# Optimization experiments

Hardware: AMD Instinct MI355X
Metric: run time of the kernel (lower is better)

The kernel has to match this reference:

```python
import jax, jax.numpy as jnp
import numpy as np
import math

N_LEVELS = 16
F_PER = 2
LOG2T = 19
TABLE = 1 << LOG2T  # 524288
BASE = 16
FINEST = 512
BANDS = 10
TIME = 0.0

_B = math.exp((math.log(FINEST) - math.log(BASE)) / (N_LEVELS - 1))
_RES = [min(int(BASE * _B ** l), FINEST) for l in range(N_LEVELS)]
# primes reduced mod table size: (c*p) mod M == (c*(p mod M)) mod M, keeps products in int32 range
_PRIMES_MOD = np.array([73856093 % TABLE, 19349663 % TABLE, 83492791 % TABLE], dtype=np.int32)
_OFFSETS = np.array([[dx, dy, dz] for dx in (0, 1) for dy in (0, 1) for dz in (0, 1)], dtype=bool)  # [8,3]


def _hash_encode(x, tables):
    # x: [N,3] in [0,1]; tables: [L, 2^19, 2]
    x = jnp.clip(x, 0.0, 1.0)
    offs = jnp.asarray(_OFFSETS)[:, None, :]  # [8,1,3]
    pm = jnp.asarray(_PRIMES_MOD)
    outs = []
    for l in range(N_LEVELS):
        res = _RES[l]
        sc = x * (res - 1)                                   # [N,3]
        cf = jnp.clip(jnp.floor(sc).astype(jnp.int32), 0, res - 1)
        cc = jnp.clip(cf + 1, 0, res - 1)
        w = sc - cf.astype(sc.dtype)                         # trilinear weights [N,3]
        corner = jnp.where(offs, cc[None], cf[None])         # [8,N,3]
        h = ((corner[..., 0] * pm[0]) % TABLE
             + (corner[..., 1] * pm[1]) % TABLE
             + (corner[..., 2] * pm[2]) % TABLE) % TABLE     # [8,N]
        feats = tables[l][h]                                 # gather [8,N,2]
        cw = jnp.prod(jnp.where(offs, w[None], 1.0 - w[None]), axis=-1)  # [8,N]
        outs.append(jnp.sum(feats * cw[..., None], axis=0))  # [N,2]
    return jnp.concatenate(outs, axis=1)                     # [N,32]


def _freq_encode(freq):
    nf = (jnp.log10(jnp.clip(freq, 1e6, 1e12)) - 6.0) / 6.0  # [N,1]
    parts = []
    for i in range(BANDS):
        a = (2.0 ** i) * math.pi * nf
        parts += [jnp.sin(a), jnp.cos(a)]
    return jnp.concatenate(parts, axis=-1)                   # [N,20]


def _ln(x, g, b, eps=1e-5):
    m = jnp.mean(x, -1, keepdims=True)
    v = jnp.var(x, -1, keepdims=True)
    return (x - m) / jnp.sqrt(v + eps) * g + b


def _forward(x, frequency, tables, W0, b0, W1, b1, W2, b2, W3, b3,
             e_w1, e_b1, e_g, e_be, e_w2, e_b2,
             m_w1, m_b1, m_g, m_be, m_w2, m_b2,
             p_w1, p_b1, p_w2, p_b2,
             mat_w1, mat_b1, mat_w2, mat_b2,
             s_w1, s_b1, s_w2, s_b2):
    pe = _hash_encode(x, tables)                             # [N,32]
    fe = _freq_encode(frequency)                             # [N,20]
    feat0 = jnp.concatenate([pe, fe], axis=1)                # [N,52]
    h = jax.nn.relu(feat0 @ W0 + b0)
    h = jax.nn.relu(h @ W1 + b1)
    h = jax.nn.relu(jnp.concatenate([h, feat0], axis=1) @ W2 + b2)  # skip connection
    h = jax.nn.relu(h @ W3 + b3)
    E_amp = jnp.tanh(jax.nn.relu(_ln(h @ e_w1 + e_b1, e_g, e_be)) @ e_w2 + e_b2)
    B_amp = jnp.tanh(jax.nn.relu(_ln(h @ m_w1 + m_b1, m_g, m_be)) @ m_w2 + m_b2)
    phases = jax.nn.relu(h @ p_w1 + p_b1) @ p_w2 + p_b2      # [N,6]
    mat = jax.nn.relu(h @ mat_w1 + mat_b1) @ mat_w2 + mat_b2 # [N,3]
    src = jax.nn.relu(h @ s_w1 + s_b1) @ s_w2 + s_b2         # [N,4]
    omega = 2.0 * math.pi * frequency                        # [N,1]
    E = E_amp * jnp.cos(omega * TIME + phases[:, :3])
    B = B_amp * jnp.cos(omega * TIME + phases[:, 3:])
    eps_r = 1.0 + jax.nn.sigmoid(mat[:, 0:1]) * 10.0
    mu_r = 1.0 + jax.nn.sigmoid(mat[:, 1:2]) * 2.0
    cond = jax.nn.sigmoid(mat[:, 2:3]) * 0.01
    # pack all float outputs: E(3) B(3) eps(1) mu(1) cond(1) charge(1) current(3)
    return jnp.concatenate([E, B, eps_r, mu_r, cond, src[:, 0:1], src[:, 1:4]], axis=1)


def _lin_init(k, fan_in, fan_out):
    k1, k2 = jax.random.split(k)
    s = 1.0 / math.sqrt(fan_in)
    W = jax.random.uniform(k1, (fan_in, fan_out), jnp.float32, -s, s)
    b = jax.random.uniform(k2, (fan_out,), jnp.float32, -s, s)
    return W, b


def setup_inputs() -> dict:
    key = jax.random.key(0)
    ks = jax.random.split(key, 20)
    N = 262144
    d = {}
    d['x'] = jax.random.uniform(ks[0], (N, 3), jnp.float32)
    d['frequency'] = 10.0 ** jax.random.uniform(ks[1], (N, 1), jnp.float32, minval=6.0, maxval=12.0)
    d['tables'] = jax.random.normal(ks[2], (N_LEVELS, TABLE, F_PER), jnp.float32) * 1e-4
    layers = [('W0', 'b0', 52, 128), ('W1', 'b1', 128, 128), ('W2', 'b2', 180, 128), ('W3', 'b3', 128, 128),
              ('e_w1', 'e_b1', 128, 64), ('e_w2', 'e_b2', 64, 3),
              ('m_w1', 'm_b1', 128, 64), ('m_w2', 'm_b2', 64, 3),
              ('p_w1', 'p_b1', 128, 32), ('p_w2', 'p_b2', 32, 6),
              ('mat_w1', 'mat_b1', 128, 64), ('mat_w2', 'mat_b2', 64, 3),
              ('s_w1', 's_b1', 128, 64), ('s_w2', 's_b2', 64, 4)]
    for j, (wn, bn, fi, fo) in enumerate(layers):
        W, b = _lin_init(jax.random.fold_in(ks[3], j), fi, fo)
        d[wn] = W
        d[bn] = b
    d['e_g'] = jnp.ones(64, jnp.float32)
    d['e_be'] = jnp.zeros(64, jnp.float32)
    d['m_g'] = jnp.ones(64, jnp.float32)
    d['m_be'] = jnp.zeros(64, jnp.float32)
    return d


def reference(x, frequency, tables, W0, b0, W1, b1, W2, b2, W3, b3,
              e_w1, e_b1, e_g, e_be, e_w2, e_b2,
              m_w1, m_b1, m_g, m_be, m_w2, m_b2,
              p_w1, p_b1, p_w2, p_b2,
              mat_w1, mat_b1, mat_w2, mat_b2,
              s_w1, s_b1, s_w2, s_b2):
    return _forward(x, frequency, tables, W0, b0, W1, b1, W2, b2, W3, b3,
                    e_w1, e_b1, e_g, e_be, e_w2, e_b2,
                    m_w1, m_b1, m_g, m_be, m_w2, m_b2,
                    p_w1, p_b1, p_w2, p_b2,
                    mat_w1, mat_b1, mat_w2, mat_b2,
                    s_w1, s_b1, s_w2, s_b2)
```

## Files before the change

kernel.cpp:

```cpp
#include <hip/hip_runtime.h>
#include <math.h>

#define TMASK 524287
#define PM0 455773
#define PM1 475295
#define PM2 130999

typedef __attribute__((ext_vector_type(8))) short bf16x8;
typedef __attribute__((ext_vector_type(4))) float f32x4;

#define OFF_W0   0
#define OFF_W1   8192
#define OFF_W2   24576
#define OFF_W3   49152
#define OFF_E    65536
#define OFF_P    81920
#define OFF_MAT  86016
#define OFF_S    94208
#define OFF_BD   102400
#define WT_TOTAL 102400
#define WT_ALLOC 111616

#define WS_TAB8_OFF (WT_ALLOC*2)
#define TAB8_BYTES  (16u*524288u*2u)
#define WS_FEAT_OFF (WS_TAB8_OFF + TAB8_BYTES)

#define TAB_SCALE   131072.0f
#define TAB_INV     (1.0f/131072.0f)

#define A6_H    0
#define A6_HL   8704
#define A6_FB   8704
#define SWF6_OFF 17408
#define LDS6_TOTAL 21712

#define SB0 0
#define SB1 128
#define SB2 256
#define SB3 384
#define SEM 512
#define SPB 640
#define SMS 672
#define SB2C 800
#define SEG 819
#define SEBE 883
#define SMG 947
#define SMBE 1011

struct Params {
  const float* x; const float* freq; const float* tables;
  const float* b0; const float* b1; const float* b2; const float* b3;
  const float* e_b1; const float* e_w2; const float* e_b2; const float* e_g; const float* e_be;
  const float* m_b1; const float* m_w2; const float* m_b2; const float* m_g; const float* m_be;
  const float* p_b1; const float* p_w2; const float* p_b2;
  const float* mat_b1; const float* mat_w2; const float* mat_b2;
  const float* s_b1; const float* s_w2; const float* s_b2;
  const short* wt;
  const unsigned* feat;
  float* out;
  int N;
  int res[16];
  const float* ssrc[18]; int sdst[18]; int scnt[18];
};

struct HashParams {
  const float* x; const unsigned short* tab8; unsigned* feat; int N; int res[16];
};
struct TabPrepParams { const float* tables; unsigned* tab8; };
struct PrepParams {
  const float* src[9];
  int end[9]; int Nsrc[9]; int Ksrc[9]; int Kpad[9];
  short* wt;
};
struct BdParams {
  const float* e; const float* m; const float* p; const float* mat; const float* s;
  short* out;
};

__device__ __forceinline__ short f2bf(float f){
  union { float f; unsigned u; } v; v.f = f;
  unsigned r = v.u + 0x7fffu + ((v.u >> 16) & 1u);
  return (short)(r >> 16);
}
__device__ __forceinline__ float bf2f(short s){
  union { unsigned u; float f; } v; v.u = ((unsigned)(unsigned short)s) << 16; return v.f;
}
__device__ __forceinline__ float sigmoid_(float v){ return 1.f/(1.f + expf(-v)); }

__global__ __launch_bounds__(256)
void prep_weights(PrepParams P)
{
  int id = blockIdx.x*256 + threadIdx.x;
  if (id >= WT_TOTAL) return;
  int r = 0, base = 0;
  #pragma unroll
  for (int i = 0; i < 9; ++i) { if (id >= P.end[i]) { r = i+1; base = P.end[i]; } }
  const int rel = id - base;
  const int kp = P.Kpad[r];
  const int n = rel / kp;
  const int k = rel - n*kp;
  float v = 0.f;
  if (k < P.Ksrc[r]) v = P.src[r][k * P.Nsrc[r] + n];
  P.wt[id] = f2bf(v);
}

__global__ __launch_bounds__(256)
void prep_bd(BdParams P)
{
  int id = blockIdx.x*256 + threadIdx.x;
  if (id >= 32*288) return;
  const int n = id / 288, k = id - n*288;
  float v = 0.f;
  if      (n < 3  && k < 64)                        v = P.e[k*3 + n];
  else if (n >= 3 && n < 6  && k >= 64  && k < 128) v = P.m[(k-64)*3 + (n-3)];
  else if (n >= 6 && n < 12 && k >= 256)            v = P.p[(k-256)*6 + (n-6)];
  else if (n >= 12&& n < 15 && k >= 128 && k < 192) v = P.mat[(k-128)*3 + (n-12)];
  else if (n >= 15&& n < 19 && k >= 192 && k < 256) v = P.s[(k-192)*4 + (n-15)];
  P.out[id] = f2bf(v);
}

__global__ __launch_bounds__(256)
void tab_prep(TabPrepParams P)
{
  const unsigned id = blockIdx.x*256 + threadIdx.x;
  if (id >= 16u*524288u/2u) return;
  const float4 v = ((const float4*)P.tables)[id];
  int q0 = (int)fminf(fmaxf(rintf(v.x*TAB_SCALE), -127.f), 127.f);
  int q1 = (int)fminf(fmaxf(rintf(v.y*TAB_SCALE), -127.f), 127.f);
  int q2 = (int)fminf(fmaxf(rintf(v.z*TAB_SCALE), -127.f), 127.f);
  int q3 = (int)fminf(fmaxf(rintf(v.w*TAB_SCALE), -127.f), 127.f);
  unsigned pack = (q0 & 255) | ((q1 & 255) << 8) | ((q2 & 255) << 16) | ((q3 & 255) << 24);
  P.tab8[id] = pack;
}

__global__ __launch_bounds__(256, 8)
void hash_encode8(HashParams P)
{
  const int b = blockIdx.x;
  const int l = b & 15;
  const int p = (b >> 4)*256 + threadIdx.x;
  if (p >= P.N) return;
  const float xs0 = fminf(fmaxf(P.x[p*3+0], 0.f), 1.f);
  const float xs1 = fminf(fmaxf(P.x[p*3+1], 0.f), 1.f);
  const float xs2 = fminf(fmaxf(P.x[p*3+2], 0.f), 1.f);
  const int res = P.res[l];
  const float rf = (float)(res-1);
  const float s0 = xs0*rf, s1 = xs1*rf, s2 = xs2*rf;
  int f0i = (int)s0; if (f0i > res-1) f0i = res-1;
  int f1i = (int)s1; if (f1i > res-1) f1i = res-1;
  int f2i = (int)s2; if (f2i > res-1) f2i = res-1;
  const float w0 = s0 - (float)f0i;
  const float w1 = s1 - (float)f1i;
  const float w2 = s2 - (float)f2i;
  int c0i = f0i+1; if (c0i > res-1) c0i = res-1;
  int c1i = f1i+1; if (c1i > res-1) c1i = res-1;
  int c2i = f2i+1; if (c2i > res-1) c2i = res-1;
  const int hx0 = (f0i*PM0) & TMASK, hx1 = (c0i*PM0) & TMASK;
  const int hy0 = (f1i*PM1) & TMASK, hy1 = (c1i*PM1) & TMASK;
  const int hz0 = (f2i*PM2) & TMASK, hz1 = (c2i*PM2) & TMASK;
  const unsigned short* tp = P.tab8 + ((size_t)l << 19);
  unsigned short tv[8];
  #pragma unroll
  for (int cn = 0; cn < 8; ++cn) {
    const int bx = (cn>>2)&1, by = (cn>>1)&1, bz = cn&1;
    const int hh = ((bx?hx1:hx0) + (by?hy1:hy0) + (bz?hz1:hz0)) & TMASK;
    tv[cn] = tp[hh];
  }
  float a0 = 0.f, a1 = 0.f;
  #pragma unroll
  for (int cn = 0; cn < 8; ++cn) {
    const int bx = (cn>>2)&1, by = (cn>>1)&1, bz = cn&1;
    const float cw = (bx?w0:1.f-w0)*(by?w1:1.f-w1)*(bz?w2:1.f-w2);
    a0 = fmaf(cw, (float)(int)(signed char)(tv[cn] & 0xff), a0);
    a1 = fmaf(cw, (float)(int)(signed char)(tv[cn] >> 8),   a1);
  }
  a0 *= TAB_INV; a1 *= TAB_INV;
  const unsigned pack = (unsigned)(unsigned short)f2bf(a0)
                      | ((unsigned)(unsigned short)f2bf(a1) << 16);
  P.feat[(size_t)p*16 + l] = pack;
}

template<int NT, int KC>
__device__ __forceinline__ void gemm32(f32x4* acc0, f32x4* acc1,
    const short* A, int lda, const short* __restrict__ wt, int kpad, int kwoff,
    int n0, int q)
{
  const short* Ap0 = A + n0*lda + q*8;
  const short* Ap1 = Ap0 + 16*lda;
  const short* Bp  = wt + n0*kpad + kwoff + q*8;
  bf16x8 bc[NT], bn[NT];
  #pragma unroll
  for (int nt = 0; nt < NT; ++nt) bc[nt] = *(const bf16x8*)(Bp + nt*16*kpad);
  #pragma unroll
  for (int kc = 0; kc < KC; ++kc) {
    if (kc + 1 < KC) {
      #pragma unroll
      for (int nt = 0; nt < NT; ++nt)
        bn[nt] = *(const bf16x8*)(Bp + nt*16*kpad + (kc+1)*32);
    }
    const bf16x8 a0 = *(const bf16x8*)(Ap0 + kc*32);
    const bf16x8 a1 = *(const bf16x8*)(Ap1 + kc*32);
    #pragma unroll
    for (int nt = 0; nt < NT; ++nt) {
      acc0[nt] = __builtin_amdgcn_mfma_f32_16x16x32_bf16(a0, bc[nt], acc0[nt], 0, 0, 0);
      acc1[nt] = __builtin_amdgcn_mfma_f32_16x16x32_bf16(a1, bc[nt], acc1[nt], 0, 0, 0);
    }
    #pragma unroll
    for (int nt = 0; nt < NT; ++nt) bc[nt] = bn[nt];
  }
}

template<int NT>
__device__ __forceinline__ void epi_trunk(const f32x4* acc0, const f32x4* acc1,
    const float* bias, short* out, int ldo, int n0, int q, int coff)
{
  #pragma unroll
  for (int nt = 0; nt < NT; ++nt) {
    const float bv = bias[nt*16 + n0];
    #pragma unroll
    for (int r = 0; r < 4; ++r) {
      float v0 = fmaxf(acc0[nt][r] + bv, 0.f);
      float v1 = fmaxf(acc1[nt][r] + bv, 0.f);
      out[(q*4 + r)*ldo + coff + nt*16 + n0]      = f2bf(v0);
      out[(16 + q*4 + r)*ldo + coff + nt*16 + n0] = f2bf(v1);
    }
  }
}

__global__ __launch_bounds__(128, 4)
void em_nerf6(Params P)
{
  __shared__ __align__(16) char smem[LDS6_TOTAL];
  const int tid = threadIdx.x;
  const int lane = tid & 63, wave = tid >> 6;
  short* H  = (short*)(smem + A6_H);
  short* HL = (short*)(smem + A6_HL);
  short* FB = (short*)(smem + A6_FB);
  float* R2 = (float*)(smem + A6_HL);
  float* swf = (float*)(smem + SWF6_OFF);
  const int n0 = lane & 15, q = lane >> 4;
  const int p0 = blockIdx.x*32;

  uint4 fv;
  { const int pl = tid >> 2, lq = tid & 3;
    int gp = p0 + pl; if (gp >= P.N) gp = P.N - 1;
    fv = *(const uint4*)(P.feat + (size_t)gp*16 + lq*4); }

  #pragma clang loop unroll(disable)
  for (int r = 0; r < 18; ++r)
    for (int i = tid; i < P.scnt[r]; i += 128) swf[P.sdst[r] + i] = P.ssrc[r][i];

  { const int pl = tid >> 2, lq = tid & 3;
    *(uint4*)&FB[pl*72 + lq*8] = fv; }

  { const int pp = tid & 31, half = tid >> 5;
    int gp = p0 + pp; if (gp >= P.N) gp = P.N - 1;
    float fr = P.freq[gp];
    fr = fminf(fmaxf(fr, 1e6f), 1e12f);
    const float nf = (log10f(fr) - 6.f) * (1.f/6.f);
    const float a0 = 3.14159274101257324f * nf;
    #pragma clang loop unroll(disable)
    for (int i = half; i < 10; i += 4) {
      const float a = a0 * (float)(1 << i);
      FB[pp*72 + 32 + 2*i] = f2bf(sinf(a));
      FB[pp*72 + 33 + 2*i] = f2bf(cosf(a));
    }
    if (half == 3) {
      #pragma unroll
      for (int k = 52; k < 64; ++k) FB[pp*72 + k] = 0;
    }
  }
  __syncthreads();

  const int ntb = wave*64;

  { f32x4 a0[4] = {}, a1[4] = {};
    gemm32<4,2>(a0, a1, FB, 72, P.wt + OFF_W0 + ntb*64, 64, 0, n0, q);
    epi_trunk<4>(a0, a1, swf + SB0 + ntb, H, 136, n0, q, ntb);
    __syncthreads(); }
  { f32x4 a0[4] = {}, a1[4] = {};
    gemm32<4,4>(a0, a1, H, 136, P.wt + OFF_W1 + ntb*128, 128, 0, n0, q);
    __syncthreads();
    epi_trunk<4>(a0, a1, swf + SB1 + ntb, H, 136, n0, q, ntb);
    __syncthreads(); }
  { f32x4 a0[4] = {}, a1[4] = {};
    gemm32<4,4>(a0, a1, H, 136, P.wt + OFF_W2 + ntb*192, 192, 0, n0, q);
    gemm32<4,2>(a0, a1, FB, 72, P.wt + OFF_W2 + ntb*192, 192, 128, n0, q);
    __syncthreads();
    epi_trunk<4>(a0, a1, swf + SB2 + ntb, H, 136, n0, q, ntb);
    __syncthreads(); }
  { f32x4 a0[4] = {}, a1[4] = {};
    gemm32<4,4>(a0, a1, H, 136, P.wt + OFF_W3 + ntb*128, 128, 0, n0, q);
    __syncthreads();
    epi_trunk<4>(a0, a1, swf + SB3 + ntb, H, 136, n0, q, ntb);
    __syncthreads(); }

  { f32x4 a0[4] = {}, a1[4] = {};
    gemm32<4,4>(a0, a1, H, 136, P.wt + OFF_E + ntb*128, 128, 0, n0, q);
    const float* bb = swf + SEM + ntb;
    #pragma unroll
    for (int nt = 0; nt < 4; ++nt) {
      const float bv = bb[nt*16 + n0];
      #pragma unroll
      for (int r = 0; r < 4; ++r) { a0[nt][r] += bv; a1[nt][r] += bv; }
    }
    float mn[2][4], iv[2][4];
    #pragma unroll
    for (int s = 0; s < 2; ++s) {
      const f32x4* A_ = s ? a1 : a0;
      #pragma unroll
      for (int r = 0; r < 4; ++r) {
        float se = 0.f, qe = 0.f;
        #pragma unroll
        for (int t = 0; t < 4; ++t) { const float x = A_[t][r]; se += x; qe = fmaf(x,x,qe); }
        #pragma unroll
        for (int msk = 1; msk < 16; msk <<= 1) {
          se += __shfl_xor(se, msk, 64);
          qe += __shfl_xor(qe, msk, 64);
        }
        const float me = se*(1.f/64.f);
        mn[s][r] = me;
        iv[s][r] = 1.f / sqrtf(qe*(1.f/64.f) - me*me + 1e-5f);
      }
    }
    const float* gg  = swf + (wave ? SMG  : SEG);
    const float* bbe = swf + (wave ? SMBE : SEBE);
    #pragma unroll
    for (int t = 0; t < 4; ++t) {
      const float g  = gg[t*16 + n0];
      const float be = bbe[t*16 + n0];
      const int col = ntb + t*16 + n0;
      #pragma unroll
      for (int s = 0; s < 2; ++s) {
        const f32x4* A_ = s ? a1 : a0;
        #pragma unroll
        for (int r = 0; r < 4; ++r) {
          float v = (A_[t][r] - mn[s][r])*iv[s][r]*g + be;
          v = fmaxf(v, 0.f);
          HL[(s*16 + q*4 + r)*136 + col] = f2bf(v);
        }
      }
    }
  }
  __syncthreads();

  f32x4 o0[1] = {}, o1[1] = {};
  gemm32<1,4>(o0, o1, HL, 136, P.wt + OFF_BD + wave*16*288, 288, 0, n0, q);

  { f32x4 a0[4] = {}, a1[4] = {};
    gemm32<4,4>(a0, a1, H, 136, P.wt + OFF_MAT + ntb*128, 128, 0, n0, q);
    __syncthreads();
    const float* bb = swf + SMS + ntb;
    #pragma unroll
    for (int t = 0; t < 4; ++t) {
      const float bv = bb[t*16 + n0];
      const int col = ntb + t*16 + n0;
      #pragma unroll
      for (int s = 0; s < 2; ++s) {
        const f32x4* A_ = s ? a1 : a0;
        #pragma unroll
        for (int r = 0; r < 4; ++r)
          HL[(s*16 + q*4 + r)*136 + col] = f2bf(fmaxf(A_[t][r] + bv, 0.f));
      }
    }
  }
  __syncthreads();

  gemm32<1,4>(o0, o1, HL, 136, P.wt + OFF_BD + wave*16*288, 288, 128, n0, q);

  { f32x4 a0[1] = {}, a1[1] = {};
    gemm32<1,4>(a0, a1, H, 136, P.wt + OFF_P + wave*16*128, 128, 0, n0, q);
    __syncthreads();
    const float bv = swf[SPB + wave*16 + n0];
    const int col = wave*16 + n0;
    #pragma unroll
    for (int s = 0; s < 2; ++s) {
      const f32x4* A_ = s ? a1 : a0;
      #pragma unroll
      for (int r = 0; r < 4; ++r)
        HL[(s*16 + q*4 + r)*136 + col] = f2bf(fmaxf(A_[s? 0:0][r] + bv, 0.f));
    }
  }
  __syncthreads();

  gemm32<1,1>(o0, o1, HL, 136, P.wt + OFF_BD + wave*16*288, 288, 256, n0, q);
  __syncthreads();

  #pragma unroll
  for (int s = 0; s < 2; ++s) {
    const f32x4* O_ = s ? o1 : o0;
    #pragma unroll
    for (int r = 0; r < 4; ++r) {
      const int p = s*16 + q*4 + r;
      if (wave == 0) {
        float v0 = O_[0][r] + swf[SB2C + n0];
        if (n0 < 6) v0 = tanhf(v0);
        R2[p*20 + n0] = v0;
      } else if (n0 < 3) {
        R2[p*20 + 16 + n0] = O_[0][r] + swf[SB2C + 16 + n0];
      }
    }
  }
  __syncthreads();

  if (tid < 32) {
    const int gp = p0 + tid;
    if (gp < P.N) {
      const float* r = R2 + tid*20;
      float* o = P.out + (size_t)gp*13;
      o[0] = r[0]*cosf(r[6]);
      o[1] = r[1]*cosf(r[7]);
      o[2] = r[2]*cosf(r[8]);
      o[3] = r[3]*cosf(r[9]);
      o[4] = r[4]*cosf(r[10]);
      o[5] = r[5]*cosf(r[11]);
      o[6] = 1.f + sigmoid_(r[12])*10.f;
      o[7] = 1.f + sigmoid_(r[13])*2.f;
      o[8] = sigmoid_(r[14])*0.01f;
      o[9]  = r[15];
      o[10] = r[16];
      o[11] = r[17];
      o[12] = r[18];
    }
  }
}

__global__ __launch_bounds__(256, 3)
void em_nerf_fallback(Params P)
{
  __shared__ __align__(16) char smem[44288];
  short* featB = (short*)smem;
  short* hA    = (short*)(smem + 9216);
  short* hB    = (short*)(smem + 9216 + 17664);
  float* headF = (float*)(smem + 9216);
  float* res2  = (float*)smem;
  __shared__ int s_res[16];

  const int tid = threadIdx.x;
  if (tid < 16) s_res[tid] = P.res[tid];
  __syncthreads();
  {
    const int p = tid & 63;
    const int g = tid >> 6;
    int gp = blockIdx.x*64 + p; if (gp >= P.N) gp = P.N - 1;
    const float xs0 = fminf(fmaxf(P.x[gp*3+0], 0.f), 1.f);
    const float xs1 = fminf(fmaxf(P.x[gp*3+1], 0.f), 1.f);
    const float xs2 = fminf(fmaxf(P.x[gp*3+2], 0.f), 1.f);
    #pragma unroll
    for (int j = 0; j < 4; ++j) {
      const int l = g*4 + j;
      const int res = s_res[l];
      const float rf = (float)(res-1);
      const float s0 = xs0*rf, s1 = xs1*rf, s2 = xs2*rf;
      int f0i = (int)s0; if (f0i > res-1) f0i = res-1;
      int f1i = (int)s1; if (f1i > res-1) f1i = res-1;
      int f2i = (int)s2; if (f2i > res-1) f2i = res-1;
      const float w0 = s0 - (float)f0i;
      const float w1 = s1 - (float)f1i;
      const float w2 = s2 - (float)f2i;
      int c0i = f0i+1; if (c0i > res-1) c0i = res-1;
      int c1i = f1i+1; if (c1i > res-1) c1i = res-1;
      int c2i = f2i+1; if (c2i > res-1) c2i = res-1;
      const int hx0 = (f0i*PM0) & TMASK, hx1 = (c0i*PM0) & TMASK;
      const int hy0 = (f1i*PM1) & TMASK, hy1 = (c1i*PM1) & TMASK;
      const int hz0 = (f2i*PM2) & TMASK, hz1 = (c2i*PM2) & TMASK;
      const float* tp = P.tables + ((size_t)l << 20);
      float a0 = 0.f, a1 = 0.f;
      #pragma unroll
      for (int cn = 0; cn < 8; ++cn) {
        const int bx = (cn>>2)&1, by = (cn>>1)&1, bz = cn&1;
        const int hh = ((bx?hx1:hx0) + (by?hy1:hy0) + (bz?hz1:hz0)) & TMASK;
        const float cw = (bx?w0:1.f-w0)*(by?w1:1.f-w1)*(bz?w2:1.f-w2);
        const float2 tv = *(const float2*)(tp + 2*hh);
        a0 = fmaf(cw, tv.x, a0);
        a1 = fmaf(cw, tv.y, a1);
      }
      featB[p*72 + 2*l]   = f2bf(a0);
      featB[p*72 + 2*l+1] = f2bf(a1);
    }
    if (g == 0) {
      float fr = P.freq[gp];
      fr = fminf(fmaxf(fr, 1e6f), 1e12f);
      const float nf = (log10f(fr) - 6.f) * (1.f/6.f);
      float a = 3.14159274101257324f * nf;
      #pragma unroll
      for (int i = 0; i < 10; ++i) {
        featB[p*72 + 32 + 2*i] = f2bf(sinf(a));
        featB[p*72 + 33 + 2*i] = f2bf(cosf(a));
        a = a * 2.f;
      }
    }
    if (g == 3) {
      #pragma unroll
      for (int k = 52; k < 64; ++k) featB[p*72 + k] = 0;
    }
  }
  __syncthreads();

  const int lane = tid & 63, wave = tid >> 6;
  const int n0 = lane & 15, q = lane >> 4;
  short* myA  = featB + wave*16*72;
  short* myH1 = hA + wave*16*136;
  short* myH2 = hB + wave*16*136;

  auto gemm1 = [&](const short* A, int lda, const short* wt, int kpad, int kwoff, int KC, f32x4* acc, int NT){
    const short* Ap = A + n0*lda + q*8;
    const short* Bp = wt + n0*kpad + kwoff + q*8;
    for (int kc = 0; kc < KC; ++kc) {
      bf16x8 a = *(const bf16x8*)(Ap + kc*32);
      for (int nt = 0; nt < NT; ++nt) {
        bf16x8 b = *(const bf16x8*)(Bp + nt*16*kpad + kc*32);
        acc[nt] = __builtin_amdgcn_mfma_f32_16x16x32_bf16(a, b, acc[nt], 0, 0, 0);
      }
    }
  };
  auto epi1 = [&](const f32x4* acc, const float* bias, short* out, int ldo, int NT, bool relu){
    for (int nt = 0; nt < NT; ++nt) {
      const float bv = bias[nt*16 + n0];
      for (int r = 0; r < 4; ++r) {
        float v = acc[nt][r] + bv;
        if (relu) v = fmaxf(v, 0.f);
        out[(q*4 + r)*ldo + nt*16 + n0] = f2bf(v);
      }
    }
  };

  { f32x4 acc[8] = {}; gemm1(myA, 72, P.wt + OFF_W0, 64, 0, 2, acc, 8);  epi1(acc, P.b0, myH1, 136, 8, true); }
  __syncthreads();
  { f32x4 acc[8] = {}; gemm1(myH1, 136, P.wt + OFF_W1, 128, 0, 4, acc, 8); epi1(acc, P.b1, myH2, 136, 8, true); }
  __syncthreads();
  { f32x4 acc[8] = {}; gemm1(myH2, 136, P.wt + OFF_W2, 192, 0, 4, acc, 8);
    gemm1(myA, 72, P.wt + OFF_W2, 192, 128, 2, acc, 8); epi1(acc, P.b2, myH1, 136, 8, true); }
  __syncthreads();
  { f32x4 acc[8] = {}; gemm1(myH1, 136, P.wt + OFF_W3, 128, 0, 4, acc, 8); epi1(acc, P.b3, myH2, 136, 8, true); }
  __syncthreads();

  float* hf = headF + wave*16*69;
  auto head1f = [&](const short* wt, const float* bias, int NT, bool relu){
    f32x4 acc[4] = {};
    gemm1(myH2, 136, wt, 128, 0, 4, acc, NT);
    for (int nt = 0; nt < NT; ++nt) {
      const float bv = bias[nt*16 + n0];
      for (int r = 0; r < 4; ++r) {
        float v = acc[nt][r] + bv;
        if (relu) v = fmaxf(v, 0.f);
        hf[(q*4 + r)*69 + nt*16 + n0] = v;
      }
    }
  };
  auto l2 = [&](int OC2, int K2, bool ln, bool th, const float* g, const float* be,
                const float* W2, const float* b2, int slot){
    __syncthreads();
    if (tid < 64) {
      const float* row = headF + tid*69;
      float mn = 0.f, iv = 1.f;
      if (ln) {
        float s = 0.f;
        for (int k = 0; k < K2; ++k) s += row[k];
        mn = s/(float)K2;
        float vv = 0.f;
        for (int k = 0; k < K2; ++k) { float d = row[k]-mn; vv = fmaf(d,d,vv); }
        iv = 1.f/sqrtf(vv/(float)K2 + 1e-5f);
      }
      for (int j = 0; j < OC2; ++j) {
        float acc = b2[j];
        for (int k = 0; k < K2; ++k) {
          float xv = row[k];
          if (ln) xv = (xv-mn)*iv*g[k] + be[k];
          xv = fmaxf(xv, 0.f);
          acc = fmaf(xv, W2[k*OC2+j], acc);
        }
        res2[tid*20 + slot + j] = th ? tanhf(acc) : acc;
      }
    }
    __syncthreads();
  };

  head1f(P.wt + OFF_E, P.e_b1, 4, false); l2(3, 64, true,  true,  P.e_g, P.e_be, P.e_w2, P.e_b2, 0);
  head1f(P.wt + OFF_E + 8192, P.m_b1, 4, false); l2(3, 64, true, true, P.m_g, P.m_be, P.m_w2, P.m_b2, 3);
  head1f(P.wt + OFF_P, P.p_b1, 2, true);  l2(6, 32, false, false, 0, 0, P.p_w2, P.p_b2, 6);
  head1f(P.wt + OFF_MAT, P.mat_b1, 4, true); l2(3, 64, false, false, 0, 0, P.mat_w2, P.mat_b2, 12);
  head1f(P.wt + OFF_S, P.s_b1, 4, true);  l2(4, 64, false, false, 0, 0, P.s_w2, P.s_b2, 15);

  if (tid < 64) {
    const int gp = blockIdx.x*64 + tid;
    if (gp < P.N) {
      const float* r = res2 + tid*20;
      float* o = P.out + (size_t)gp*13;
      o[0] = r[0]*cosf(r[6]);
      o[1] = r[1]*cosf(r[7]);
      o[2] = r[2]*cosf(r[8]);
      o[3] = r[3]*cosf(r[9]);
      o[4] = r[4]*cosf(r[10]);
      o[5] = r[5]*cosf(r[11]);
      o[6] = 1.f + sigmoid_(r[12])*10.f;
      o[7] = 1.f + sigmoid_(r[13])*2.f;
      o[8] = sigmoid_(r[14])*0.01f;
      o[9]  = r[15];
      o[10] = r[16];
      o[11] = r[17];
      o[12] = r[18];
    }
  }
}

extern "C" void kernel_launch(void* const* d_in, const int* in_sizes, int n_in,
                              void* d_out, int out_size, void* d_ws, size_t ws_size,
                              hipStream_t stream) {
  (void)n_in; (void)out_size;
  const float** in = (const float**)d_in;
  const int N = in_sizes[0] / 3;

  PrepParams PP;
  const float* srcs[9] = { in[3], in[5], in[7], in[9], in[11], in[15], in[19], in[23], in[27] };
  const int ends[9]  = { 8192, 24576, 49152, 65536, 73728, 81920, 86016, 94208, 102400 };
  const int nsrc[9]  = { 128, 128, 128, 128, 64, 64, 32, 64, 64 };
  const int ksrc[9]  = { 52, 128, 180, 128, 128, 128, 128, 128, 128 };
  const int kpad[9]  = { 64, 128, 192, 128, 128, 128, 128, 128, 128 };
  for (int i = 0; i < 9; ++i) { PP.src[i]=srcs[i]; PP.end[i]=ends[i]; PP.Nsrc[i]=nsrc[i]; PP.Ksrc[i]=ksrc[i]; PP.Kpad[i]=kpad[i]; }
  PP.wt = (short*)d_ws;
  hipLaunchKernelGGL(prep_weights, dim3((WT_TOTAL+255)/256), dim3(256), 0, stream, PP);

  BdParams BP;
  BP.e = in[13]; BP.m = in[17]; BP.p = in[21]; BP.mat = in[25]; BP.s = in[29];
  BP.out = (short*)d_ws + OFF_BD;
  hipLaunchKernelGGL(prep_bd, dim3((32*288 + 255)/256), dim3(256), 0, stream, BP);

  Params P;
  P.x = in[0]; P.freq = in[1]; P.tables = in[2];
  P.b0 = in[4]; P.b1 = in[6]; P.b2 = in[8]; P.b3 = in[10];
  P.e_b1 = in[12]; P.e_w2 = in[13]; P.e_b2 = in[14];
  P.m_b1 = in[16]; P.m_w2 = in[17]; P.m_b2 = in[18];
  P.p_b1 = in[20]; P.p_w2 = in[21]; P.p_b2 = in[22];
  P.mat_b1 = in[24]; P.mat_w2 = in[25]; P.mat_b2 = in[26];
  P.s_b1 = in[28]; P.s_w2 = in[29]; P.s_b2 = in[30];
  P.e_g = in[31]; P.e_be = in[32]; P.m_g = in[33]; P.m_be = in[34];
  P.wt = (const short*)d_ws;
  P.feat = (const unsigned*)((const char*)d_ws + WS_FEAT_OFF);
  P.out = (float*)d_out;
  P.N = N;

  const float* ssrc[18] = { in[4], in[6], in[8], in[10],
                            in[12], in[16], in[20], in[24], in[28],
                            in[14], in[18], in[22], in[26], in[30],
                            in[31], in[32], in[33], in[34] };
  const int sdst[18] = { 0,128,256,384, 512,576,640,672,736, 800,803,806,812,815, 819,883,947,1011 };
  const int scnt[18] = { 128,128,128,128, 64,64,32,64,64, 3,3,6,3,4, 64,64,64,64 };
  for (int i = 0; i < 18; ++i) { P.ssrc[i]=ssrc[i]; P.sdst[i]=sdst[i]; P.scnt[i]=scnt[i]; }

  const double B = exp((log(512.0) - log(16.0)) / 15.0);
  for (int l = 0; l < 16; ++l) {
    double r = 16.0 * pow(B, (double)l);
    int ri = (int)r;
    if (ri > 512) ri = 512;
    P.res[l] = ri;
  }

  const size_t need = (size_t)WS_FEAT_OFF + (size_t)N*16*4;

  if (ws_size >= need) {
    TabPrepParams TP;
    TP.tables = in[2];
    TP.tab8 = (unsigned*)((char*)d_ws + WS_TAB8_OFF);
    hipLaunchKernelGGL(tab_prep, dim3((16*524288/2 + 255)/256), dim3(256), 0, stream, TP);

    HashParams HP;
    HP.x = in[0];
    HP.tab8 = (const unsigned short*)((const char*)d_ws + WS_TAB8_OFF);
    HP.feat = (unsigned*)((char*)d_ws + WS_FEAT_OFF);
    HP.N = N;
    for (int l = 0; l < 16; ++l) HP.res[l] = P.res[l];
    const int chunks = (N + 255) / 256;
    hipLaunchKernelGGL(hash_encode8, dim3(chunks*16), dim3(256), 0, stream, HP);

    hipLaunchKernelGGL(em_nerf6, dim3((N + 31) / 32), dim3(128), 0, stream, P);
  } else {
    hipLaunchKernelGGL(em_nerf_fallback, dim3((N + 63) / 64), dim3(256), 0, stream, P);
  }
}
```

Before: 539.3 us.

## Fuse hash-grid encoding into the MLP kernel and drop the feature buffer

```diff
diff --git a/kernel.cpp b/kernel.cpp
--- a/kernel.cpp
+++ b/kernel.cpp
@@ -23,7 +23,6 @@
 
 #define WS_TAB8_OFF (WT_ALLOC*2)
 #define TAB8_BYTES  (16u*524288u*2u)
-#define WS_FEAT_OFF (WS_TAB8_OFF + TAB8_BYTES)
 
 #define TAB_SCALE   131072.0f
 #define TAB_INV     (1.0f/131072.0f)
@@ -56,16 +55,13 @@
   const float* mat_b1; const float* mat_w2; const float* mat_b2;
   const float* s_b1; const float* s_w2; const float* s_b2;
   const short* wt;
-  const unsigned* feat;
+  const unsigned short* tab8;
   float* out;
   int N;
   int res[16];
   const float* ssrc[18]; int sdst[18]; int scnt[18];
 };
 
-struct HashParams {
-  const float* x; const unsigned short* tab8; unsigned* feat; int N; int res[16];
-};
 struct TabPrepParams { const float* tables; unsigned* tab8; };
 struct PrepParams {
   const float* src[9];
@@ -133,53 +129,6 @@
   P.tab8[id] = pack;
 }
 
-__global__ __launch_bounds__(256, 8)
-void hash_encode8(HashParams P)
-{
-  const int b = blockIdx.x;
-  const int l = b & 15;
-  const int p = (b >> 4)*256 + threadIdx.x;
-  if (p >= P.N) return;
-  const float xs0 = fminf(fmaxf(P.x[p*3+0], 0.f), 1.f);
-  const float xs1 = fminf(fmaxf(P.x[p*3+1], 0.f), 1.f);
-  const float xs2 = fminf(fmaxf(P.x[p*3+2], 0.f), 1.f);
-  const int res = P.res[l];
-  const float rf = (float)(res-1);
-  const float s0 = xs0*rf, s1 = xs1*rf, s2 = xs2*rf;
-  int f0i = (int)s0; if (f0i > res-1) f0i = res-1;
-  int f1i = (int)s1; if (f1i > res-1) f1i = res-1;
-  int f2i = (int)s2; if (f2i > res-1) f2i = res-1;
-  const float w0 = s0 - (float)f0i;
-  const float w1 = s1 - (float)f1i;
-  const float w2 = s2 - (float)f2i;
-  int c0i = f0i+1; if (c0i > res-1) c0i = res-1;
-  int c1i = f1i+1; if (c1i > res-1) c1i = res-1;
-  int c2i = f2i+1; if (c2i > res-1) c2i = res-1;
-  const int hx0 = (f0i*PM0) & TMASK, hx1 = (c0i*PM0) & TMASK;
-  const int hy0 = (f1i*PM1) & TMASK, hy1 = (c1i*PM1) & TMASK;
-  const int hz0 = (f2i*PM2) & TMASK, hz1 = (c2i*PM2) & TMASK;
-  const unsigned short* tp = P.tab8 + ((size_t)l << 19);
-  unsigned short tv[8];
-  #pragma unroll
-  for (int cn = 0; cn < 8; ++cn) {
-    const int bx = (cn>>2)&1, by = (cn>>1)&1, bz = cn&1;
-    const int hh = ((bx?hx1:hx0) + (by?hy1:hy0) + (bz?hz1:hz0)) & TMASK;
-    tv[cn] = tp[hh];
-  }
-  float a0 = 0.f, a1 = 0.f;
-  #pragma unroll
-  for (int cn = 0; cn < 8; ++cn) {
-    const int bx = (cn>>2)&1, by = (cn>>1)&1, bz = cn&1;
-    const float cw = (bx?w0:1.f-w0)*(by?w1:1.f-w1)*(bz?w2:1.f-w2);
-    a0 = fmaf(cw, (float)(int)(signed char)(tv[cn] & 0xff), a0);
-    a1 = fmaf(cw, (float)(int)(signed char)(tv[cn] >> 8),   a1);
-  }
-  a0 *= TAB_INV; a1 *= TAB_INV;
-  const unsigned pack = (unsigned)(unsigned short)f2bf(a0)
-                      | ((unsigned)(unsigned short)f2bf(a1) << 16);
-  P.feat[(size_t)p*16 + l] = pack;
-}
-
 template<int NT, int KC>
 __device__ __forceinline__ void gemm32(f32x4* acc0, f32x4* acc1,
     const short* A, int lda, const short* __restrict__ wt, int kpad, int kwoff,
@@ -228,7 +177,7 @@
 }
 
 __global__ __launch_bounds__(128, 4)
-void em_nerf6(Params P)
+void em_nerf7(Params P)
 {
   __shared__ __align__(16) char smem[LDS6_TOTAL];
   const int tid = threadIdx.x;
@@ -241,34 +190,83 @@
   const int n0 = lane & 15, q = lane >> 4;
   const int p0 = blockIdx.x*32;
 
-  uint4 fv;
-  { const int pl = tid >> 2, lq = tid & 3;
-    int gp = p0 + pl; if (gp >= P.N) gp = P.N - 1;
-    fv = *(const uint4*)(P.feat + (size_t)gp*16 + lq*4); }
+  const int pp = tid & 31;
+  const int lbase = tid >> 5;
+  int gp = p0 + pp; if (gp >= P.N) gp = P.N - 1;
+  const float xs0 = fminf(fmaxf(P.x[gp*3+0], 0.f), 1.f);
+  const float xs1 = fminf(fmaxf(P.x[gp*3+1], 0.f), 1.f);
+  const float xs2 = fminf(fmaxf(P.x[gp*3+2], 0.f), 1.f);
+  const float frq = P.freq[gp];
+
+  unsigned short tv[4][8];
+  float W0w[4], W1w[4], W2w[4];
+  #pragma unroll
+  for (int lg = 0; lg < 4; ++lg) {
+    const int l = lbase + lg*4;
+    static const int RT[16] = {16,20,25,32,40,50,64,80,101,128,161,203,256,322,406,512};
+    const int r0 = RT[lg*4+0], r1 = RT[lg*4+1], r2 = RT[lg*4+2], r3 = RT[lg*4+3];
+    const int lo = (lbase & 1) ? r1 : r0;
+    const int hi = (lbase & 1) ? r3 : r2;
+    const int res = (lbase & 2) ? hi : lo;
+    const float rf = (float)(res-1);
+    const float s0 = xs0*rf, s1 = xs1*rf, s2 = xs2*rf;
+    int f0i = (int)s0; if (f0i > res-1) f0i = res-1;
+    int f1i = (int)s1; if (f1i > res-1) f1i = res-1;
+    int f2i = (int)s2; if (f2i > res-1) f2i = res-1;
+    W0w[lg] = s0 - (float)f0i;
+    W1w[lg] = s1 - (float)f1i;
+    W2w[lg] = s2 - (float)f2i;
+    int c0i = f0i+1; if (c0i > res-1) c0i = res-1;
+    int c1i = f1i+1; if (c1i > res-1) c1i = res-1;
+    int c2i = f2i+1; if (c2i > res-1) c2i = res-1;
+    const int hx0 = (f0i*PM0) & TMASK, hx1 = (c0i*PM0) & TMASK;
+    const int hy0 = (f1i*PM1) & TMASK, hy1 = (c1i*PM1) & TMASK;
+    const int hz0 = (f2i*PM2) & TMASK, hz1 = (c2i*PM2) & TMASK;
+    const unsigned lb = ((unsigned)l << 19);
+    #pragma unroll
+    for (int cn = 0; cn < 8; ++cn) {
+      const int bx = (cn>>2)&1, by = (cn>>1)&1, bz = cn&1;
+      const unsigned hh = (unsigned)(((bx?hx1:hx0) + (by?hy1:hy0) + (bz?hz1:hz0)) & TMASK);
+      tv[lg][cn] = P.tab8[lb + hh];
+    }
+  }
 
   #pragma clang loop unroll(disable)
   for (int r = 0; r < 18; ++r)
     for (int i = tid; i < P.scnt[r]; i += 128) swf[P.sdst[r] + i] = P.ssrc[r][i];
 
-  { const int pl = tid >> 2, lq = tid & 3;
-    *(uint4*)&FB[pl*72 + lq*8] = fv; }
-
-  { const int pp = tid & 31, half = tid >> 5;
-    int gp = p0 + pp; if (gp >= P.N) gp = P.N - 1;
-    float fr = P.freq[gp];
-    fr = fminf(fmaxf(fr, 1e6f), 1e12f);
+  {
+    float fr = fminf(fmaxf(frq, 1e6f), 1e12f);
     const float nf = (log10f(fr) - 6.f) * (1.f/6.f);
     const float a0 = 3.14159274101257324f * nf;
     #pragma clang loop unroll(disable)
-    for (int i = half; i < 10; i += 4) {
+    for (int i = lbase; i < 10; i += 4) {
       const float a = a0 * (float)(1 << i);
       FB[pp*72 + 32 + 2*i] = f2bf(sinf(a));
       FB[pp*72 + 33 + 2*i] = f2bf(cosf(a));
     }
-    if (half == 3) {
+    if (lbase == 3) {
       #pragma unroll
       for (int k = 52; k < 64; ++k) FB[pp*72 + k] = 0;
     }
+  }
+
+  #pragma unroll
+  for (int lg = 0; lg < 4; ++lg) {
+    const int l = lbase + lg*4;
+    const float w0 = W0w[lg], w1 = W1w[lg], w2 = W2w[lg];
+    float a0 = 0.f, a1 = 0.f;
+    #pragma unroll
+    for (int cn = 0; cn < 8; ++cn) {
+      const int bx = (cn>>2)&1, by = (cn>>1)&1, bz = cn&1;
+      const float cw = (bx?w0:1.f-w0)*(by?w1:1.f-w1)*(bz?w2:1.f-w2);
+      a0 = fmaf(cw, (float)(int)(signed char)(tv[lg][cn] & 0xff), a0);
+      a1 = fmaf(cw, (float)(int)(signed char)(tv[lg][cn] >> 8),   a1);
+    }
+    a0 *= TAB_INV; a1 *= TAB_INV;
+    const unsigned pack = (unsigned)(unsigned short)f2bf(a0)
+                        | ((unsigned)(unsigned short)f2bf(a1) << 16);
+    *(unsigned*)&FB[pp*72 + 2*l] = pack;
   }
   __syncthreads();
 
@@ -378,7 +376,7 @@
       const f32x4* A_ = s ? a1 : a0;
       #pragma unroll
       for (int r = 0; r < 4; ++r)
-        HL[(s*16 + q*4 + r)*136 + col] = f2bf(fmaxf(A_[s? 0:0][r] + bv, 0.f));
+        HL[(s*16 + q*4 + r)*136 + col] = f2bf(fmaxf(A_[0][r] + bv, 0.f));
     }
   }
   __syncthreads();
@@ -404,10 +402,10 @@
   __syncthreads();
 
   if (tid < 32) {
-    const int gp = p0 + tid;
-    if (gp < P.N) {
+    const int gp2 = p0 + tid;
+    if (gp2 < P.N) {
       const float* r = R2 + tid*20;
-      float* o = P.out + (size_t)gp*13;
+      float* o = P.out + (size_t)gp2*13;
       o[0] = r[0]*cosf(r[6]);
       o[1] = r[1]*cosf(r[7]);
       o[2] = r[2]*cosf(r[8]);
@@ -636,7 +634,7 @@
   P.s_b1 = in[28]; P.s_w2 = in[29]; P.s_b2 = in[30];
   P.e_g = in[31]; P.e_be = in[32]; P.m_g = in[33]; P.m_be = in[34];
   P.wt = (const short*)d_ws;
-  P.feat = (const unsigned*)((const char*)d_ws + WS_FEAT_OFF);
+  P.tab8 = (const unsigned short*)((const char*)d_ws + WS_TAB8_OFF);
   P.out = (float*)d_out;
   P.N = N;
 
@@ -656,7 +654,7 @@
     P.res[l] = ri;
   }
 
-  const size_t need = (size_t)WS_FEAT_OFF + (size_t)N*16*4;
+  const size_t need = (size_t)WS_TAB8_OFF + (size_t)TAB8_BYTES;
 
   if (ws_size >= need) {
     TabPrepParams TP;
@@ -664,16 +662,7 @@
     TP.tab8 = (unsigned*)((char*)d_ws + WS_TAB8_OFF);
     hipLaunchKernelGGL(tab_prep, dim3((16*524288/2 + 255)/256), dim3(256), 0, stream, TP);
 
-    HashParams HP;
-    HP.x = in[0];
-    HP.tab8 = (const unsigned short*)((const char*)d_ws + WS_TAB8_OFF);
-    HP.feat = (unsigned*)((char*)d_ws + WS_FEAT_OFF);
-    HP.N = N;
-    for (int l = 0; l < 16; ++l) HP.res[l] = P.res[l];
-    const int chunks = (N + 255) / 256;
-    hipLaunchKernelGGL(hash_encode8, dim3(chunks*16), dim3(256), 0, stream, HP);
-
-    hipLaunchKernelGGL(em_nerf6, dim3((N + 31) / 32), dim3(128), 0, stream, P);
+    hipLaunchKernelGGL(em_nerf7, dim3((N + 31) / 32), dim3(128), 0, stream, P);
   } else {
     hipLaunchKernelGGL(em_nerf_fallback, dim3((N + 63) / 64), dim3(256), 0, stream, P);
   }
```

New measurement: 704.5 us. +30.6%, slower.

## Densify coarse hash levels into LDS-resident grids for level 0-3 encoding

Applied to the files above, without the earlier changes.

```diff
diff --git a/kernel.cpp b/kernel.cpp
--- a/kernel.cpp
+++ b/kernel.cpp
@@ -24,6 +24,7 @@
 #define WS_TAB8_OFF (WT_ALLOC*2)
 #define TAB8_BYTES  (16u*524288u*2u)
 #define WS_FEAT_OFF (WS_TAB8_OFF + TAB8_BYTES)
+#define DENSE_BYTES 120992
 
 #define TAB_SCALE   131072.0f
 #define TAB_INV     (1.0f/131072.0f)
@@ -66,6 +67,10 @@
 struct HashParams {
   const float* x; const unsigned short* tab8; unsigned* feat; int N; int res[16];
 };
+struct CoarseParams {
+  const float* x; const unsigned short* dense; unsigned* feat; int N;
+};
+struct DensePrepParams { const unsigned short* tab8; unsigned short* dense; };
 struct TabPrepParams { const float* tables; unsigned* tab8; };
 struct PrepParams {
   const float* src[9];
@@ -133,11 +138,83 @@
   P.tab8[id] = pack;
 }
 
+__global__ __launch_bounds__(256)
+void dense_prep(DensePrepParams P)
+{
+  const int id = blockIdx.x*256 + threadIdx.x;
+  const int l = id >> 15;
+  const int c = id & 32767;
+  const int RT4[4] = {16,20,25,32};
+  const unsigned DOFFU[4] = {0, 4096, 12096, 27728};
+  const int res = RT4[l];
+  if (c >= res*res*res) return;
+  const int cz = c % res;
+  const int t  = c / res;
+  const int cy = t % res;
+  const int cx = t / res;
+  const unsigned h = (unsigned)((cx*PM0 + cy*PM1 + cz*PM2) & TMASK);
+  P.dense[DOFFU[l] + c] = P.tab8[((unsigned)l << 19) + h];
+}
+
+__global__ __launch_bounds__(256)
+void hash_coarse(CoarseParams P)
+{
+  __shared__ unsigned short tabl[32768];
+  const int b = blockIdx.x;
+  const int l = b & 3;
+  const int chunk = b >> 2;
+  const int tid = threadIdx.x;
+  const int RT4[4] = {16,20,25,32};
+  const unsigned DOFFU[4] = {0, 4096, 12096, 27728};
+  const int SG16[4] = {512, 1000, 1954, 4096};
+  const int res = RT4[l];
+  { const uint4* src = (const uint4*)(P.dense + DOFFU[l]);
+    const int n16 = SG16[l];
+    for (int i = tid; i < n16; i += 256) ((uint4*)tabl)[i] = src[i]; }
+  __syncthreads();
+  #pragma clang loop unroll(disable)
+  for (int it = 0; it < 4; ++it) {
+    const int p = chunk*1024 + it*256 + tid;
+    if (p >= P.N) break;
+    const float xs0 = fminf(fmaxf(P.x[p*3+0], 0.f), 1.f);
+    const float xs1 = fminf(fmaxf(P.x[p*3+1], 0.f), 1.f);
+    const float xs2 = fminf(fmaxf(P.x[p*3+2], 0.f), 1.f);
+    const float rf = (float)(res-1);
+    const float s0 = xs0*rf, s1 = xs1*rf, s2 = xs2*rf;
+    int f0i = (int)s0; if (f0i > res-1) f0i = res-1;
+    int f1i = (int)s1; if (f1i > res-1) f1i = res-1;
+    int f2i = (int)s2; if (f2i > res-1) f2i = res-1;
+    const float w0 = s0 - (float)f0i;
+    const float w1 = s1 - (float)f1i;
+    const float w2 = s2 - (float)f2i;
+    int c0i = f0i+1; if (c0i > res-1) c0i = res-1;
+    int c1i = f1i+1; if (c1i > res-1) c1i = res-1;
+    int c2i = f2i+1; if (c2i > res-1) c2i = res-1;
+    const int sx0 = f0i*res*res, sx1 = c0i*res*res;
+    const int ty0 = f1i*res,     ty1 = c1i*res;
+    float a0 = 0.f, a1 = 0.f;
+    #pragma unroll
+    for (int cn = 0; cn < 8; ++cn) {
+      const int bx = (cn>>2)&1, by = (cn>>1)&1, bz = cn&1;
+      const int idx = (bx?sx1:sx0) + (by?ty1:ty0) + (bz?c2i:f2i);
+      const unsigned short tvv = tabl[idx];
+      const float cw = (bx?w0:1.f-w0)*(by?w1:1.f-w1)*(bz?w2:1.f-w2);
+      a0 = fmaf(cw, (float)(int)(signed char)(tvv & 0xff), a0);
+      a1 = fmaf(cw, (float)(int)(signed char)(tvv >> 8),   a1);
+    }
+    a0 *= TAB_INV; a1 *= TAB_INV;
+    const unsigned pack = (unsigned)(unsigned short)f2bf(a0)
+                        | ((unsigned)(unsigned short)f2bf(a1) << 16);
+    P.feat[(size_t)p*16 + l] = pack;
+  }
+}
+
 __global__ __launch_bounds__(256, 8)
 void hash_encode8(HashParams P)
 {
   const int b = blockIdx.x;
   const int l = b & 15;
+  if (l < 4) return;
   const int p = (b >> 4)*256 + threadIdx.x;
   if (p >= P.N) return;
   const float xs0 = fminf(fmaxf(P.x[p*3+0], 0.f), 1.f);
@@ -378,7 +455,7 @@
       const f32x4* A_ = s ? a1 : a0;
       #pragma unroll
       for (int r = 0; r < 4; ++r)
-        HL[(s*16 + q*4 + r)*136 + col] = f2bf(fmaxf(A_[s? 0:0][r] + bv, 0.f));
+        HL[(s*16 + q*4 + r)*136 + col] = f2bf(fmaxf(A_[0][r] + bv, 0.f));
     }
   }
   __syncthreads();
@@ -656,13 +733,29 @@
     P.res[l] = ri;
   }
 
-  const size_t need = (size_t)WS_FEAT_OFF + (size_t)N*16*4;
+  const size_t feat_bytes = (size_t)N*16*4;
+  const size_t need = (size_t)WS_FEAT_OFF + feat_bytes + DENSE_BYTES;
 
   if (ws_size >= need) {
     TabPrepParams TP;
     TP.tables = in[2];
     TP.tab8 = (unsigned*)((char*)d_ws + WS_TAB8_OFF);
     hipLaunchKernelGGL(tab_prep, dim3((16*524288/2 + 255)/256), dim3(256), 0, stream, TP);
+
+    char* dense_base = (char*)d_ws + WS_FEAT_OFF + feat_bytes;
+
+    DensePrepParams DP;
+    DP.tab8 = (const unsigned short*)((const char*)d_ws + WS_TAB8_OFF);
+    DP.dense = (unsigned short*)dense_base;
+    hipLaunchKernelGGL(dense_prep, dim3(4*32768/256), dim3(256), 0, stream, DP);
+
+    CoarseParams CP;
+    CP.x = in[0];
+    CP.dense = (const unsigned short*)dense_base;
+    CP.feat = (unsigned*)((char*)d_ws + WS_FEAT_OFF);
+    CP.N = N;
+    const int cchunks = (N + 1023) / 1024;
+    hipLaunchKernelGGL(hash_coarse, dim3(cchunks*4), dim3(256), 0, stream, CP);
 
     HashParams HP;
     HP.x = in[0];
```

Result: slower. 564.0 us (+4.6%).
